# Kernel tuning notes

Hardware: AMD Instinct MI355X
Metric: run time of the kernel (lower is better)

The kernel has to match this reference:

```python
import jax, jax.numpy as jnp
import numpy as np

NUM_LEVELS = 4
RADIUS = 4


def avg_pool2(x):
    # x: [N, H, W] -> [N, H//2, W//2] (kernel 2, stride 2 average pool)
    n, h, w = x.shape
    return x.reshape(n, h // 2, 2, w // 2, 2).mean(axis=(2, 4))


def bilinear_sample(img, x, y):
    # img: [N, H, W]; x, y: [N, S, S] absolute pixel coords (align_corners=True),
    # zero padding outside [0, W-1] x [0, H-1] (matches F.grid_sample defaults).
    n, h, w = img.shape
    x0 = jnp.floor(x)
    y0 = jnp.floor(y)
    wx1 = x - x0
    wy1 = y - y0
    wx0 = 1.0 - wx1
    wy0 = 1.0 - wy1
    nidx = jnp.arange(n)[:, None, None]

    def gather(yi, xi):
        valid = (xi >= 0) & (xi <= w - 1) & (yi >= 0) & (yi <= h - 1)
        xic = jnp.clip(xi, 0, w - 1).astype(jnp.int32)
        yic = jnp.clip(yi, 0, h - 1).astype(jnp.int32)
        return jnp.where(valid, img[nidx, yic, xic], 0.0)

    return (gather(y0, x0) * wy0 * wx0 + gather(y0, x0 + 1) * wy0 * wx1
            + gather(y0 + 1, x0) * wy1 * wx0 + gather(y0 + 1, x0 + 1) * wy1 * wx1)


def setup_inputs() -> dict:
    key = jax.random.key(0)
    k1, k2, k3 = jax.random.split(key, 3)
    b, c, h, w = 2, 256, 64, 64
    fmap1 = jax.random.normal(k1, (b, c, h, w), dtype=jnp.float32)
    fmap2 = jax.random.normal(k2, (b, c, h, w), dtype=jnp.float32)
    # absolute pixel (x, y) coordinates in [0, W-1] / [0, H-1]
    centroids_coords = jax.random.uniform(k3, (b, 2, h, w), dtype=jnp.float32) * (w - 1)
    return {"fmap1": fmap1, "fmap2": fmap2, "centroids_coords": centroids_coords}


def reference(fmap1, fmap2, centroids_coords):
    b, c, h1, w1 = fmap1.shape
    h2, w2 = fmap2.shape[-2:]
    # correlation volume: [b, h1*w1, h2*w2] / sqrt(c)
    f1 = fmap1.reshape(b, c, h1 * w1)
    f2 = fmap2.reshape(b, c, h2 * w2)
    corr = jnp.einsum('bcm,bcn->bmn', f1, f2) / jnp.sqrt(jnp.asarray(c, fmap1.dtype))
    corr = corr.reshape(b * h1 * w1, h2, w2)

    pyramid = [corr]
    for _ in range(NUM_LEVELS - 1):
        corr = avg_pool2(corr)
        pyramid.append(corr)

    side = 2 * RADIUS + 1
    di = jnp.linspace(-RADIUS, RADIUS, side)
    # delta[..., 0] = di (added to x), delta[..., 1] = dj (added to y) -- as in source
    delta = jnp.stack(jnp.meshgrid(di, di, indexing='ij'), axis=-1)  # [S, S, 2]

    cc = centroids_coords.transpose(0, 2, 3, 1).reshape(b * h1 * w1, 1, 1, 2)
    feats = []
    for lvl, vol in enumerate(pyramid):
        grid = cc / (2.0 ** lvl) + delta[None]  # [N, S, S, 2]
        sampled = bilinear_sample(vol, grid[..., 0], grid[..., 1])  # [N, S, S]
        feats.append(sampled.reshape(b, h1, w1, side * side))
    # [b, num_levels*side^2, h1, w1]
    return jnp.concatenate(feats, axis=-1).transpose(0, 3, 1, 2)
```

## Files before the change

kernel.cpp:

```cpp
#include <hip/hip_runtime.h>
#include <stdint.h>

#define M_DIM 4096
#define K_DIM 256

typedef unsigned short us;
typedef __attribute__((ext_vector_type(8))) short bf16x8;
typedef __attribute__((ext_vector_type(4))) float f32x4;

static __device__ __forceinline__ float bf2f(unsigned int u){
  unsigned int x = u << 16; float f;
  __builtin_memcpy(&f, &x, 4); return f;
}
static __device__ __forceinline__ us f2bf(float f){
  unsigned int x; __builtin_memcpy(&x, &f, 4);
  unsigned int r = x + 0x7fffu + ((x >> 16) & 1u);
  return (us)(r >> 16);
}
static __device__ __forceinline__ void gld16(const void* g, void* l){
  __builtin_amdgcn_global_load_lds(
      (const __attribute__((address_space(1))) unsigned int*)g,
      (__attribute__((address_space(3))) unsigned int*)l, 16, 0, 0);
}

__global__ void k_transpose_cast(const float* __restrict__ f1,
                                 const float* __restrict__ f2,
                                 us* __restrict__ A, us* __restrict__ B0){
  __shared__ float lds[64][65];
  int z = blockIdx.z;
  int b = z & 1, which = z >> 1;
  const float* in = which ? f2 : f1;
  us* out = which ? B0 : A;
  float scale = which ? 1.0f : 0.0625f;
  int c0 = blockIdx.y * 64, m0 = blockIdx.x * 64;
  const float* ib = in + (size_t)b * K_DIM * M_DIM;
  us* ob = out + (size_t)b * M_DIM * K_DIM;
  int t = threadIdx.x, r = t >> 6, j = t & 63;
#pragma unroll
  for (int k = 0; k < 16; k++)
    lds[r + k*4][j] = ib[(size_t)(c0 + r + k*4) * M_DIM + m0 + j];
  __syncthreads();
#pragma unroll
  for (int k = 0; k < 16; k++)
    ob[(size_t)(m0 + r + k*4) * K_DIM + c0 + j] = f2bf(lds[j][r + k*4] * scale);
}

__global__ void k_pool_all(const us* __restrict__ B0, us* __restrict__ B1,
                           us* __restrict__ B2, us* __restrict__ B3){
  int bid = blockIdx.x;
  us* dst; int wd, f;
  if (bid < 512)      { dst = B1; wd = 32; f = 2; }
  else if (bid < 640) { bid -= 512; dst = B2; wd = 16; f = 4; }
  else                { bid -= 640; dst = B3; wd = 8;  f = 8; }
  int t = threadIdx.x;
  int idx = bid * 4 + (t >> 6);
  int l = t & 63;
  int per = wd * wd;
  int b = idx / per, rem = idx - b * per;
  int y = rem / wd, x = rem - y * wd;
  const us* sb = B0 + (size_t)b * 4096 * K_DIM;
  float s0 = 0, s1 = 0, s2 = 0, s3 = 0;
  for (int dy = 0; dy < f; dy++)
    for (int dx = 0; dx < f; dx++){
      size_t off = ((size_t)(f*y + dy) * 64 + (f*x + dx)) * K_DIM + l * 4;
      uint2 v = *(const uint2*)(sb + off);
      s0 += bf2f(v.x & 0xffff); s1 += bf2f(v.x >> 16);
      s2 += bf2f(v.y & 0xffff); s3 += bf2f(v.y >> 16);
    }
  float inv = 1.0f / (float)(f * f);
  uint2 o;
  o.x = (unsigned)f2bf(s0*inv) | ((unsigned)f2bf(s1*inv) << 16);
  o.y = (unsigned)f2bf(s2*inv) | ((unsigned)f2bf(s3*inv) << 16);
  us* db = dst + (size_t)b * per * K_DIM;
  *(uint2*)(db + (size_t)rem * K_DIM + l * 4) = o;
}

__global__ __launch_bounds__(256) void k_corr_taps(
    const us* __restrict__ A,
    const us* __restrict__ B0, const us* __restrict__ B1,
    const us* __restrict__ B2, const us* __restrict__ B3,
    const float* __restrict__ cc, float* __restrict__ taps){
  __shared__ __align__(16) us As[4096];
  __shared__ __align__(16) us Bs[4096];
  __shared__ unsigned meta[128];
  int bx = blockIdx.x, b = blockIdx.z, m0 = blockIdx.y * 128;
  int lvl, ntiles, n0c;
  const us* B;
  if (bx < 8)       { lvl = 0; B = B0; ntiles = 4; n0c = bx * 512; }
  else if (bx < 10) { lvl = 1; B = B1; ntiles = 4; n0c = (bx - 8) * 512; }
  else if (bx == 10){ lvl = 2; B = B2; ntiles = 2; n0c = 0; }
  else              { lvl = 3; B = B3; ntiles = 1; n0c = 0; }
  int wl = 64 >> lvl, lsh = 6 - lvl, N = wl * wl;
  float inv = 1.0f / (float)(1 << lvl);
  int t = threadIdx.x;

  if (t < 128){
    int m = m0 + t;
    float cx = cc[(size_t)b * 8192 + m];
    float cy = cc[(size_t)b * 8192 + 4096 + m];
    int px0 = (int)floorf(cx * inv) - 4;
    int py0 = (int)floorf(cy * inv) - 4;
    meta[t] = ((unsigned)(py0 + 8) << 16) | (unsigned)(px0 + 8);
  }

  const us* Ab = A + (size_t)b * M_DIM * K_DIM;
  const us* Bb = B + (size_t)b * N * K_DIM;
  float* tb = taps + (size_t)(b * 4 + lvl) * 4096 * 128;
  int wave = t >> 6, lane = t & 63;
  int wm = (wave >> 1) * 64, wn = (wave & 1) * 64;
  int srow = t >> 2, scol = (t & 3) * 8;
  int fr = lane & 15, fk = (lane >> 4) * 8;
  int cr = (lane >> 4) * 4, ccol = lane & 15;
  const us* ga0 = Ab + (size_t)(m0 + srow) * K_DIM + scol;
  const us* ga1 = ga0 + (size_t)64 * K_DIM;

  for (int tile = 0; tile < ntiles; ++tile){
    int n0 = n0c + tile * 128;
    int nr0 = n0 + srow;      if (nr0 > N - 1) nr0 = N - 1;
    int nr1 = n0 + srow + 64; if (nr1 > N - 1) nr1 = N - 1;
    const us* gb0 = Bb + (size_t)nr0 * K_DIM + scol;
    const us* gb1 = Bb + (size_t)nr1 * K_DIM + scol;

    f32x4 acc[4][4];
#pragma unroll
    for (int i = 0; i < 4; i++)
#pragma unroll
      for (int j = 0; j < 4; j++) acc[i][j] = (f32x4){0.f, 0.f, 0.f, 0.f};

    for (int kt = 0; kt < K_DIM; kt += 32){
      __syncthreads();
      gld16(ga0 + kt, As + t * 8);
      gld16(ga1 + kt, As + t * 8 + 2048);
      gld16(gb0 + kt, Bs + t * 8);
      gld16(gb1 + kt, Bs + t * 8 + 2048);
      asm volatile("s_waitcnt vmcnt(0)" ::: "memory");
      __syncthreads();
      bf16x8 af[4], bfv[4];
#pragma unroll
      for (int i = 0; i < 4; i++)
        af[i] = *(const bf16x8*)(As + (wm + i*16 + fr) * 32 + fk);
#pragma unroll
      for (int j = 0; j < 4; j++)
        bfv[j] = *(const bf16x8*)(Bs + (wn + j*16 + fr) * 32 + fk);
#pragma unroll
      for (int i = 0; i < 4; i++)
#pragma unroll
        for (int j = 0; j < 4; j++)
          acc[i][j] = __builtin_amdgcn_mfma_f32_16x16x32_bf16(af[i], bfv[j], acc[i][j], 0, 0, 0);
    }

#pragma unroll
    for (int i = 0; i < 4; i++){
#pragma unroll
      for (int r = 0; r < 4; r++){
        int lrow = wm + i*16 + cr + r;
        unsigned mv = meta[lrow];
        int px0 = (int)(mv & 0xffffu) - 8;
        int py0 = (int)(mv >> 16) - 8;
        float* pb = tb + (size_t)(m0 + lrow) * 128;
#pragma unroll
        for (int j = 0; j < 4; j++){
          int col = n0 + wn + j*16 + ccol;
          int y2 = col >> lsh, x2 = col & (wl - 1);
          int dy = y2 - py0, dx = x2 - px0;
          if ((unsigned)dy < 10u && (unsigned)dx < 10u && col < N)
            pb[dy * 10 + dx] = acc[i][j][r];
        }
      }
    }
  }
}

__global__ __launch_bounds__(256) void k_combine(
    const float* __restrict__ taps, const float* __restrict__ cc,
    float* __restrict__ out){
  __shared__ float T[128 * 129];
  int m0 = blockIdx.x * 128, b = blockIdx.y, lvl = blockIdx.z;
  int t = threadIdx.x;
  const float* src = taps + ((size_t)(b * 4 + lvl) * 4096 + m0) * 128;
  for (int k = t; k < 16384; k += 256)
    T[(k >> 7) * 129 + (k & 127)] = src[k];
  __syncthreads();

  int px = t & 127, half = t >> 7;
  int m = m0 + px;
  float inv = 1.0f / (float)(1 << lvl);
  float cx = cc[(size_t)b * 8192 + m];
  float cy = cc[(size_t)b * 8192 + 4096 + m];
  float xs = cx * inv, ys = cy * inv;
  float fx = xs - floorf(xs), fy = ys - floorf(ys);
  float wx1 = fx, wx0 = 1.0f - fx, wy1 = fy, wy0 = 1.0f - fy;
  const float* Tp = &T[px * 129];
  size_t ob = ((size_t)b * 324 + lvl * 81) * 4096 + m;
  int o_lo = half ? 41 : 0, o_hi = half ? 81 : 41;
#pragma unroll
  for (int a = 0; a < 9; a++)
#pragma unroll
    for (int d = 0; d < 9; d++){
      int o = a * 9 + d;
      if (o >= o_lo && o < o_hi){
        float s = wy0 * (wx0 * Tp[d*10 + a]     + wx1 * Tp[d*10 + a + 1])
                + wy1 * (wx0 * Tp[(d+1)*10 + a] + wx1 * Tp[(d+1)*10 + a + 1]);
        out[ob + (size_t)o * 4096] = s;
      }
    }
}

extern "C" void kernel_launch(void* const* d_in, const int* in_sizes, int n_in,
                              void* d_out, int out_size, void* d_ws, size_t ws_size,
                              hipStream_t stream){
  (void)in_sizes; (void)n_in; (void)out_size; (void)ws_size;
  const float* f1 = (const float*)d_in[0];
  const float* f2 = (const float*)d_in[1];
  const float* cc = (const float*)d_in[2];
  float* out = (float*)d_out;
  char* ws = (char*)d_ws;
  us* A  = (us*)(ws + 0);
  us* B0 = (us*)(ws + 4194304);
  us* B1 = (us*)(ws + 8388608);
  us* B2 = (us*)(ws + 9437184);
  us* B3 = (us*)(ws + 9699328);
  float* taps = (float*)(ws + 9764864);

  k_transpose_cast<<<dim3(64, 4, 4), dim3(256), 0, stream>>>(f1, f2, A, B0);
  k_pool_all<<<dim3(672), dim3(256), 0, stream>>>(B0, B1, B2, B3);
  hipMemsetAsync(taps, 0, (size_t)2 * 4 * 4096 * 128 * 4, stream);
  k_corr_taps<<<dim3(12, 32, 2), dim3(256), 0, stream>>>(A, B0, B1, B2, B3, cc, taps);
  k_combine<<<dim3(32, 2, 4), dim3(256), 0, stream>>>(taps, cc, out);
}
```

Baseline: 164.4 us.

## Split corr tiles across more blocks and drop taps memset via masked combine reads

The correlation kernel now gives each block a single 128-column tile, with 43 blocks along x instead of 12, so a block no longer loops over up to four tiles and the grid exposes more parallelism. The memset that zeroed the 16 MB taps buffer is removed. In its place, the combine kernel recomputes each pixel's window origin and reads only in-bounds taps, writing zero for out-of-image slots. This removes a large memory-write pass, but the A tile is now reloaded once per block instead of being shared across several N tiles.

Result: faster. 159.8 us (-2.8%).

```diff
diff --git a/kernel.cpp b/kernel.cpp
--- a/kernel.cpp
+++ b/kernel.cpp
@@ -84,12 +84,12 @@
   __shared__ __align__(16) us Bs[4096];
   __shared__ unsigned meta[128];
   int bx = blockIdx.x, b = blockIdx.z, m0 = blockIdx.y * 128;
-  int lvl, ntiles, n0c;
+  int lvl, n0;
   const us* B;
-  if (bx < 8)       { lvl = 0; B = B0; ntiles = 4; n0c = bx * 512; }
-  else if (bx < 10) { lvl = 1; B = B1; ntiles = 4; n0c = (bx - 8) * 512; }
-  else if (bx == 10){ lvl = 2; B = B2; ntiles = 2; n0c = 0; }
-  else              { lvl = 3; B = B3; ntiles = 1; n0c = 0; }
+  if (bx < 32)      { lvl = 0; B = B0; n0 = bx * 128; }
+  else if (bx < 40) { lvl = 1; B = B1; n0 = (bx - 32) * 128; }
+  else if (bx < 42) { lvl = 2; B = B2; n0 = (bx - 40) * 128; }
+  else              { lvl = 3; B = B3; n0 = 0; }
   int wl = 64 >> lvl, lsh = 6 - lvl, N = wl * wl;
   float inv = 1.0f / (float)(1 << lvl);
   int t = threadIdx.x;
@@ -111,61 +111,61 @@
   int srow = t >> 2, scol = (t & 3) * 8;
   int fr = lane & 15, fk = (lane >> 4) * 8;
   int cr = (lane >> 4) * 4, ccol = lane & 15;
+  int nr0 = n0 + srow;      if (nr0 > N - 1) nr0 = N - 1;
+  int nr1 = n0 + srow + 64; if (nr1 > N - 1) nr1 = N - 1;
   const us* ga0 = Ab + (size_t)(m0 + srow) * K_DIM + scol;
   const us* ga1 = ga0 + (size_t)64 * K_DIM;
-
-  for (int tile = 0; tile < ntiles; ++tile){
-    int n0 = n0c + tile * 128;
-    int nr0 = n0 + srow;      if (nr0 > N - 1) nr0 = N - 1;
-    int nr1 = n0 + srow + 64; if (nr1 > N - 1) nr1 = N - 1;
-    const us* gb0 = Bb + (size_t)nr0 * K_DIM + scol;
-    const us* gb1 = Bb + (size_t)nr1 * K_DIM + scol;
-
-    f32x4 acc[4][4];
+  const us* gb0 = Bb + (size_t)nr0 * K_DIM + scol;
+  const us* gb1 = Bb + (size_t)nr1 * K_DIM + scol;
+
+  f32x4 acc[4][4];
+#pragma unroll
+  for (int i = 0; i < 4; i++)
+#pragma unroll
+    for (int j = 0; j < 4; j++) acc[i][j] = (f32x4){0.f, 0.f, 0.f, 0.f};
+
+  for (int kt = 0; kt < K_DIM; kt += 32){
+    __syncthreads();
+    gld16(ga0 + kt, As + t * 8);
+    gld16(ga1 + kt, As + t * 8 + 2048);
+    gld16(gb0 + kt, Bs + t * 8);
+    gld16(gb1 + kt, Bs + t * 8 + 2048);
+    asm volatile("s_waitcnt vmcnt(0)" ::: "memory");
+    __syncthreads();
+    bf16x8 af[4], bfv[4];
 #pragma unroll
     for (int i = 0; i < 4; i++)
-#pragma unroll
-      for (int j = 0; j < 4; j++) acc[i][j] = (f32x4){0.f, 0.f, 0.f, 0.f};
-
-    for (int kt = 0; kt < K_DIM; kt += 32){
-      __syncthreads();
-      gld16(ga0 + kt, As + t * 8);
-      gld16(ga1 + kt, As + t * 8 + 2048);
-      gld16(gb0 + kt, Bs + t * 8);
-      gld16(gb1 + kt, Bs + t * 8 + 2048);
-      asm volatile("s_waitcnt vmcnt(0)" ::: "memory");
-      __syncthreads();
-      bf16x8 af[4], bfv[4];
-#pragma unroll
-      for (int i = 0; i < 4; i++)
-        af[i] = *(const bf16x8*)(As + (wm + i*16 + fr) * 32 + fk);
+      af[i] = *(const bf16x8*)(As + (wm + i*16 + fr) * 32 + fk);
+#pragma unroll
+    for (int j = 0; j < 4; j++)
+      bfv[j] = *(const bf16x8*)(Bs + (wn + j*16 + fr) * 32 + fk);
+#pragma unroll
+    for (int i = 0; i < 4; i++)
 #pragma unroll
       for (int j = 0; j < 4; j++)
-        bfv[j] = *(const bf16x8*)(Bs + (wn + j*16 + fr) * 32 + fk);
-#pragma unroll
-      for (int i = 0; i < 4; i++)
-#pragma unroll
-        for (int j = 0; j < 4; j++)
-          acc[i][j] = __builtin_amdgcn_mfma_f32_16x16x32_bf16(af[i], bfv[j], acc[i][j], 0, 0, 0);
-    }
-
-#pragma unroll
-    for (int i = 0; i < 4; i++){
-#pragma unroll
-      for (int r = 0; r < 4; r++){
-        int lrow = wm + i*16 + cr + r;
-        unsigned mv = meta[lrow];
-        int px0 = (int)(mv & 0xffffu) - 8;
-        int py0 = (int)(mv >> 16) - 8;
-        float* pb = tb + (size_t)(m0 + lrow) * 128;
-#pragma unroll
-        for (int j = 0; j < 4; j++){
-          int col = n0 + wn + j*16 + ccol;
-          int y2 = col >> lsh, x2 = col & (wl - 1);
-          int dy = y2 - py0, dx = x2 - px0;
-          if ((unsigned)dy < 10u && (unsigned)dx < 10u && col < N)
-            pb[dy * 10 + dx] = acc[i][j][r];
-        }
+        acc[i][j] = __builtin_amdgcn_mfma_f32_16x16x32_bf16(af[i], bfv[j], acc[i][j], 0, 0, 0);
+  }
+
+  int y2j[4], x2j[4]; bool cokj[4];
+#pragma unroll
+  for (int j = 0; j < 4; j++){
+    int col = n0 + wn + j*16 + ccol;
+    y2j[j] = col >> lsh; x2j[j] = col & (wl - 1); cokj[j] = col < N;
+  }
+#pragma unroll
+  for (int i = 0; i < 4; i++){
+#pragma unroll
+    for (int r = 0; r < 4; r++){
+      int lrow = wm + i*16 + cr + r;
+      unsigned mv = meta[lrow];
+      int px0 = (int)(mv & 0xffffu) - 8;
+      int py0 = (int)(mv >> 16) - 8;
+      float* pb = tb + (size_t)(m0 + lrow) * 128;
+#pragma unroll
+      for (int j = 0; j < 4; j++){
+        int dy = y2j[j] - py0, dx = x2j[j] - px0;
+        if (cokj[j] && (unsigned)dy < 10u && (unsigned)dx < 10u)
+          pb[dy * 10 + dx] = acc[i][j][r];
       }
     }
   }
@@ -175,16 +175,41 @@
     const float* __restrict__ taps, const float* __restrict__ cc,
     float* __restrict__ out){
   __shared__ float T[128 * 129];
+  __shared__ unsigned meta[128];
   int m0 = blockIdx.x * 128, b = blockIdx.y, lvl = blockIdx.z;
   int t = threadIdx.x;
+  int wl = 64 >> lvl;
+  float inv = 1.0f / (float)(1 << lvl);
+
+  if (t < 128){
+    int m = m0 + t;
+    float cx = cc[(size_t)b * 8192 + m];
+    float cy = cc[(size_t)b * 8192 + 4096 + m];
+    int px0 = (int)floorf(cx * inv) - 4;
+    int py0 = (int)floorf(cy * inv) - 4;
+    meta[t] = ((unsigned)(py0 + 8) << 16) | (unsigned)(px0 + 8);
+  }
+  __syncthreads();
+
   const float* src = taps + ((size_t)(b * 4 + lvl) * 4096 + m0) * 128;
-  for (int k = t; k < 16384; k += 256)
-    T[(k >> 7) * 129 + (k & 127)] = src[k];
+  int slot = t & 127;
+  if (slot < 100){
+    int dy = slot / 10, dx = slot - dy * 10;
+#pragma unroll
+    for (int it = 0; it < 64; it++){
+      int p = (t >> 7) + 2 * it;
+      unsigned mv = meta[p];
+      int px0 = (int)(mv & 0xffffu) - 8;
+      int py0 = (int)(mv >> 16) - 8;
+      bool ok = ((unsigned)(py0 + dy) < (unsigned)wl) &&
+                ((unsigned)(px0 + dx) < (unsigned)wl);
+      T[p * 129 + slot] = ok ? src[(size_t)p * 128 + slot] : 0.0f;
+    }
+  }
   __syncthreads();
 
   int px = t & 127, half = t >> 7;
   int m = m0 + px;
-  float inv = 1.0f / (float)(1 << lvl);
   float cx = cc[(size_t)b * 8192 + m];
   float cy = cc[(size_t)b * 8192 + 4096 + m];
   float xs = cx * inv, ys = cy * inv;
@@ -224,7 +249,6 @@
 
   k_transpose_cast<<<dim3(64, 4, 4), dim3(256), 0, stream>>>(f1, f2, A, B0);
   k_pool_all<<<dim3(672), dim3(256), 0, stream>>>(B0, B1, B2, B3);
-  hipMemsetAsync(taps, 0, (size_t)2 * 4 * 4096 * 128 * 4, stream);
-  k_corr_taps<<<dim3(12, 32, 2), dim3(256), 0, stream>>>(A, B0, B1, B2, B3, cc, taps);
+  k_corr_taps<<<dim3(43, 32, 2), dim3(256), 0, stream>>>(A, B0, B1, B2, B3, cc, taps);
   k_combine<<<dim3(32, 2, 4), dim3(256), 0, stream>>>(taps, cc, out);
 }
```
